# Kernel tuning notes

Measured on AMD Instinct MI355X. Metric: run time of the kernel, lower is better.

## Reference

```python
import jax, jax.numpy as jnp
import numpy as np

N, L, S, C, H = 8, 1024, 1024, 512, 8
SCALE = float((C // H) ** 0.5)  # sqrt(64), as in source (based on embed_dim, not cat'd dim)


def _linear_params(key, c_in, c_out):
    kw, kb = jax.random.split(key)
    lim = 1.0 / np.sqrt(c_in)
    W = jax.random.uniform(kw, (c_out, c_in), jnp.float32, -lim, lim)
    b = jax.random.uniform(kb, (c_out,), jnp.float32, -lim, lim)
    return W, b


def setup_inputs() -> dict:
    key = jax.random.key(0)
    ks = jax.random.split(key, 12)
    inp = {
        'q_c': jax.random.normal(ks[0], (N, L, C), jnp.float32),
        'q_p': jax.random.normal(ks[1], (N, L, C), jnp.float32),
        'k_c': jax.random.normal(ks[2], (N, S, C), jnp.float32),
        'k_p': jax.random.normal(ks[3], (N, S, C), jnp.float32),
        'v': jax.random.normal(ks[4], (N, S, C), jnp.float32),
        'attn_mask': jax.random.normal(ks[5], (N, H, L, S), jnp.float32),
    }
    for i, name in enumerate(['qc', 'qp', 'kc', 'kp', 'v', 'o']):
        W, b = _linear_params(ks[6 + i], C, C)
        inp[f'W_{name}'] = W
        inp[f'b_{name}'] = b
    return inp


def _split_head(x, h):
    n, l, c = x.shape
    return x.reshape(n, l, h, c // h).transpose(0, 2, 1, 3)  # (N,H,L,c/h)


def reference(q_c, q_p, k_c, k_p, v, attn_mask,
              W_qc, b_qc, W_qp, b_qp, W_kc, b_kc, W_kp, b_kp, W_v, b_v, W_o, b_o):
    # dual projections + cat -> (N, L, 2C)
    q = jnp.concatenate([q_c @ W_qc.T + b_qc, q_p @ W_qp.T + b_qp], axis=-1)
    k = jnp.concatenate([k_c @ W_kc.T + b_kc, k_p @ W_kp.T + b_kp], axis=-1)
    vv = v @ W_v.T + b_v
    q = _split_head(q, H)   # (N,H,L,2C/H)
    k = _split_head(k, H)   # (N,H,S,2C/H)
    vv = _split_head(vv, H)  # (N,H,S,C/H)
    attn = jnp.einsum('nhld,nhsd->nhls', q / SCALE, k) + attn_mask
    attn = jax.nn.softmax(attn, axis=-1)
    out = jnp.einsum('nhls,nhsd->nhld', attn, vv)
    out = out.transpose(0, 2, 1, 3).reshape(N, L, C)
    return out @ W_o.T + b_o
```

## Files before the change

### kernel.cpp

```cpp
#include <hip/hip_runtime.h>
#include <hip/hip_bf16.h>

typedef __bf16 bf16;
typedef __bf16 bf16x8 __attribute__((ext_vector_type(8)));
typedef float  f32x4  __attribute__((ext_vector_type(4)));
typedef float  f32x2  __attribute__((ext_vector_type(2)));

#define LOG2E        1.4426950408889634f
#define QSCALE_LOG2E 0.18033688011112043f
#define DEFER_THR    20.0f

#define GLDS(g, l)                                                        \
  __builtin_amdgcn_global_load_lds(                                       \
      (const __attribute__((address_space(1))) void*)(g),                 \
      (__attribute__((address_space(3))) void*)(l), 16, 0, 0)

#define WAITV(n) asm volatile("s_waitcnt vmcnt(" #n ")" ::: "memory")
#define BARRIER() do {                                                    \
  __builtin_amdgcn_s_barrier();                                           \
  __builtin_amdgcn_sched_barrier(0);                                      \
} while (0)

__device__ __forceinline__ void stage_f32_tile(const float* __restrict__ src, int ld,
                                               char* dst, int tid) {
  #pragma unroll
  for (int t = 0; t < 8; ++t) {
    int c8  = tid + t * 256;
    int row = c8 >> 4;
    int h8  = c8 & 15;
    const f32x4 v = *reinterpret_cast<const f32x4*>(src + row * ld + h8 * 4);
    union { bf16 h[4]; unsigned long long u; } pk;
    pk.h[0] = (bf16)v[0]; pk.h[1] = (bf16)v[1];
    pk.h[2] = (bf16)v[2]; pk.h[3] = (bf16)v[3];
    int byte = (row << 7) + ((((h8 >> 1) ^ (row & 7)) << 4) | ((h8 & 1) << 3));
    *reinterpret_cast<unsigned long long*>(dst + byte) = pk.u;
  }
}

__device__ __forceinline__ void stage_bf16_tile(const bf16* __restrict__ src, int ld,
                                                char* dst, int tid) {
  #pragma unroll
  for (int t = 0; t < 4; ++t) {
    int c   = tid + t * 256;
    int row = c >> 3;
    int ck  = c & 7;
    const bf16x8 v = *reinterpret_cast<const bf16x8*>(src + row * ld + ck * 8);
    int byte = (row << 7) + (((ck ^ (row & 7)) << 4));
    *reinterpret_cast<bf16x8*>(dst + byte) = v;
  }
}

__global__ __launch_bounds__(256) void proj_gemm(
    const float* __restrict__ qc, const float* __restrict__ qp,
    const float* __restrict__ kc, const float* __restrict__ kp,
    const float* __restrict__ vin,
    const float* __restrict__ Wqc, const float* __restrict__ bqc,
    const float* __restrict__ Wqp, const float* __restrict__ bqp,
    const float* __restrict__ Wkc, const float* __restrict__ bkc,
    const float* __restrict__ Wkp, const float* __restrict__ bkp,
    const float* __restrict__ Wv,  const float* __restrict__ bv,
    bf16* __restrict__ Qws, bf16* __restrict__ Kws, bf16* __restrict__ Vtws) {
  __shared__ __align__(16) bf16 lA[128 * 64];
  __shared__ __align__(16) bf16 lB[128 * 64];
  char* lAb = (char*)lA;
  char* lBb = (char*)lB;

  const int bxr = blockIdx.x;
  const int bx  = (bxr & 7) * 160 + (bxr >> 3);
  const int g  = bx >> 8;
  const int mt = (bx & 255) >> 2;
  const int nt = bx & 3;

  const float *A, *W, *bias;
  if      (g == 0) { A = qc;  W = Wqc; bias = bqc; }
  else if (g == 1) { A = qp;  W = Wqp; bias = bqp; }
  else if (g == 2) { A = kc;  W = Wkc; bias = bkc; }
  else if (g == 3) { A = kp;  W = Wkp; bias = bkp; }
  else             { A = vin; W = Wv;  bias = bv;  }

  const int tid  = threadIdx.x;
  const int lane = tid & 63, wid = tid >> 6;
  const int wr = wid >> 1, wc = wid & 1;
  const int lrow = lane & 15, lgrp = lane >> 4;

  const float* Abase = A + (size_t)(mt * 128) * 512;
  const float* Wbase = W + (size_t)(nt * 128) * 512;

  const f32x4 fz = {0.f, 0.f, 0.f, 0.f};
  f32x4 acc[4][4];
  #pragma unroll
  for (int i = 0; i < 4; ++i)
    #pragma unroll
    for (int j = 0; j < 4; ++j) acc[i][j] = fz;

  for (int k0 = 0; k0 < 512; k0 += 64) {
    __syncthreads();
    stage_f32_tile(Abase + k0, 512, lAb, tid);
    stage_f32_tile(Wbase + k0, 512, lBb, tid);
    __syncthreads();
    #pragma unroll
    for (int kk = 0; kk < 2; ++kk) {
      bf16x8 af[4], bfr[4];
      #pragma unroll
      for (int mf = 0; mf < 4; ++mf) {
        int row  = wr * 64 + mf * 16 + lrow;
        int byte = (row << 7) + ((((kk << 2) | lgrp) ^ (row & 7)) << 4);
        af[mf] = *reinterpret_cast<const bf16x8*>(lAb + byte);
      }
      #pragma unroll
      for (int nf = 0; nf < 4; ++nf) {
        int row  = wc * 64 + nf * 16 + lrow;
        int byte = (row << 7) + ((((kk << 2) | lgrp) ^ (row & 7)) << 4);
        bfr[nf] = *reinterpret_cast<const bf16x8*>(lBb + byte);
      }
      #pragma unroll
      for (int mf = 0; mf < 4; ++mf)
        #pragma unroll
        for (int nf = 0; nf < 4; ++nf)
          acc[mf][nf] = __builtin_amdgcn_mfma_f32_16x16x32_bf16(
              af[mf], bfr[nf], acc[mf][nf], 0, 0, 0);
    }
  }

  float bcol[4];
  #pragma unroll
  for (int nf = 0; nf < 4; ++nf)
    bcol[nf] = bias[nt * 128 + wc * 64 + nf * 16 + lrow];

  #pragma unroll
  for (int mf = 0; mf < 4; ++mf) {
    #pragma unroll
    for (int nf = 0; nf < 4; ++nf) {
      #pragma unroll
      for (int r = 0; r < 4; ++r) {
        int grow = mt * 128 + wr * 64 + mf * 16 + lgrp * 4 + r;
        int col  = nt * 128 + wc * 64 + nf * 16 + lrow;
        float vv = acc[mf][nf][r] + bcol[nf];
        bf16 hb  = (bf16)vv;
        int n = grow >> 10, tt = grow & 1023;
        if (g < 2) {
          int j = (g << 9) + col;
          Qws[(size_t)((((n << 3) + (j >> 7)) << 10) | tt) * 128 + (j & 127)] = hb;
        } else if (g < 4) {
          int j = ((g - 2) << 9) + col;
          Kws[(size_t)((((n << 3) + (j >> 7)) << 10) | tt) * 128 + (j & 127)] = hb;
        } else {
          int h = col >> 6, d = col & 63;
          Vtws[(size_t)((((n << 3) + h) << 6) + d) * 1024 + tt] = hb;
        }
      }
    }
  }
}

__global__ __launch_bounds__(256) void attn_fwd(
    const bf16* __restrict__ Qws, const bf16* __restrict__ Kws,
    const bf16* __restrict__ Vtws, const float* __restrict__ mask,
    bf16* __restrict__ Ows) {
  __shared__ __align__(16) char Kl[2][8192];
  __shared__ __align__(16) char Vl[2][4096];
  __shared__ __align__(16) char Ml[5][8192];
  __shared__ __align__(16) char Pl[4][1024];

  const int bxr = blockIdx.x;
  const int bx  = (bxr & 7) * 128 + (bxr >> 3);
  const int nh = bx >> 4;
  const int qt = bx & 15;
  const int tid = threadIdx.x;
  const int lane = tid & 63, wid = tid >> 6;
  const int lrow = lane & 15, lgrp = lane >> 4;
  const int q0 = qt * 64 + wid * 16;

  const bf16* Qb = Qws + ((size_t)(nh * 1024 + q0 + lrow)) * 128 + lgrp * 8;
  bf16x8 qf[4];
  #pragma unroll
  for (int kk = 0; kk < 4; ++kk)
    qf[kk] = *reinterpret_cast<const bf16x8*>(Qb + kk * 32);

  const float* Mblk = mask + ((size_t)(nh * 1024) + qt * 64) * 1024;
  const float* Mg = Mblk + (size_t)(lane >> 3) * 1024 +
                    (((lane & 7) ^ (lane >> 3)) << 2);

  const bf16* sgp[4];
  char* sdp[4];
  int srcMul = 128, dstStride = 8192;
  if (wid == 1 || wid == 2) {
    #pragma unroll
    for (int jj = 0; jj < 4; ++jj) {
      int j = (wid - 1) * 4 + jj;
      int c = j * 64 + lane;
      int key = c >> 4, kd = c & 15;
      sgp[jj] = Kws + ((size_t)(nh * 1024 + key)) * 128 + (kd ^ ((key >> 1) & 7)) * 8;
      sdp[jj] = (char*)&Kl[0][0] + j * 1024;
    }
  } else if (wid == 3) {
    #pragma unroll
    for (int jj = 0; jj < 4; ++jj) {
      int c = jj * 64 + lane;
      int vr = c >> 2, vs = c & 3;
      sgp[jj] = Vtws + ((size_t)(nh * 64 + vr)) * 1024 + vs * 8;
      sdp[jj] = (char*)&Vl[0][0] + jj * 1024;
    }
    srcMul = 1; dstStride = 4096;
  }

  char* Pb = &Pl[wid][0];

  const f32x4 fz = {0.f, 0.f, 0.f, 0.f};
  f32x4 oacc[4];
  #pragma unroll
  for (int dt = 0; dt < 4; ++dt) oacc[dt] = fz;
  float m2[4], lsum[4];
  #pragma unroll
  for (int r = 0; r < 4; ++r) { m2[r] = 0.f; lsum[r] = 0.f; }

  auto stageM = [&](char* dst, int sN) {
    #pragma unroll
    for (int i = 0; i < 8; ++i)
      GLDS(Mg + i * 8192 + sN, dst + i * 1024);
  };
  auto stageKV = [&](int buf, int sN) {
    if (wid >= 1) {
      #pragma unroll
      for (int jj = 0; jj < 4; ++jj)
        GLDS(sgp[jj] + (size_t)sN * srcMul, sdp[jj] + buf * dstStride);
    }
  };

  auto compute = [&](const char* Kb, const char* Vb, const char* Mb) {
    bf16x8 kf0[4], kf1[4], vf[4];
    #pragma unroll
    for (int kk = 0; kk < 4; ++kk) {
      int cb = ((((kk << 2) | lgrp) ^ (lrow & 7)) << 4);
      kf0[kk] = *reinterpret_cast<const bf16x8*>(Kb + lrow * 512 + cb);
      kf1[kk] = *reinterpret_cast<const bf16x8*>(Kb + lrow * 512 + 256 + cb);
    }
    #pragma unroll
    for (int dt = 0; dt < 4; ++dt)
      vf[dt] = *reinterpret_cast<const bf16x8*>(Vb + (dt * 16 + lrow) * 64 + lgrp * 16);
    f32x2 mk[4];
    #pragma unroll
    for (int r = 0; r < 4; ++r) {
      int qrow = wid * 16 + lgrp * 4 + r;
      int mchunk = (lrow >> 1) ^ (qrow & 7);
      mk[r] = *reinterpret_cast<const f32x2*>(
          Mb + qrow * 128 + (mchunk << 4) + ((lrow & 1) << 3));
    }

    f32x4 sc0 = fz, sc1 = fz;
    __builtin_amdgcn_s_setprio(1);
    #pragma unroll
    for (int kk = 0; kk < 4; ++kk)
      sc0 = __builtin_amdgcn_mfma_f32_16x16x32_bf16(qf[kk], kf0[kk], sc0, 0, 0, 0);
    #pragma unroll
    for (int kk = 0; kk < 4; ++kk)
      sc1 = __builtin_amdgcn_mfma_f32_16x16x32_bf16(qf[kk], kf1[kk], sc1, 0, 0, 0);
    __builtin_amdgcn_s_setprio(0);

    float a0r[4], a1r[4];
    bool ok = true;
    #pragma unroll
    for (int r = 0; r < 4; ++r) {
      a0r[r] = fmaf(sc0[r], QSCALE_LOG2E, mk[r].x * LOG2E);
      a1r[r] = fmaf(sc1[r], QSCALE_LOG2E, mk[r].y * LOG2E);
      ok &= (fmaxf(a0r[r], a1r[r]) <= m2[r] + DEFER_THR);
    }
    if (__builtin_expect(!__all(ok), 0)) {
      #pragma unroll
      for (int r = 0; r < 4; ++r) {
        float tv = fmaxf(a0r[r], a1r[r]);
        tv = fmaxf(tv, __shfl_xor(tv, 1));
        tv = fmaxf(tv, __shfl_xor(tv, 2));
        tv = fmaxf(tv, __shfl_xor(tv, 4));
        tv = fmaxf(tv, __shfl_xor(tv, 8));
        float mn = fmaxf(m2[r], tv);
        float corr = exp2f(m2[r] - mn);
        m2[r] = mn;
        lsum[r] *= corr;
        #pragma unroll
        for (int dt = 0; dt < 4; ++dt) oacc[dt][r] *= corr;
      }
    }
    #pragma unroll
    for (int r = 0; r < 4; ++r) {
      float e0 = exp2f(a0r[r] - m2[r]);
      float e1 = exp2f(a1r[r] - m2[r]);
      lsum[r] += e0 + e1;
      union { bf16 h[2]; unsigned u; } pk;
      pk.h[0] = (bf16)e0; pk.h[1] = (bf16)e1;
      int row = lgrp * 4 + r;
      int byte = row * 64 + ((((lrow >> 2) ^ (row & 3)) << 4) | ((lrow & 3) << 2));
      *reinterpret_cast<unsigned*>(Pb + byte) = pk.u;
    }
    __builtin_amdgcn_wave_barrier();
    __builtin_amdgcn_sched_barrier(0);
    bf16x8 pf = *reinterpret_cast<const bf16x8*>(
        Pb + lrow * 64 + ((lgrp ^ (lrow & 3)) << 4));

    __builtin_amdgcn_s_setprio(1);
    #pragma unroll
    for (int dt = 0; dt < 4; ++dt)
      oacc[dt] = __builtin_amdgcn_mfma_f32_16x16x32_bf16(pf, vf[dt], oacc[dt], 0, 0, 0);
    __builtin_amdgcn_s_setprio(0);
  };

  char *mr0 = &Ml[0][0], *mr1 = &Ml[1][0], *mr2 = &Ml[2][0],
       *mr3 = &Ml[3][0], *mr4 = &Ml[4][0];
  auto rotM = [&]() {
    char* tp = mr0; mr0 = mr1; mr1 = mr2; mr2 = mr3; mr3 = mr4; mr4 = tp;
  };

  if (wid == 0) {
    stageM(mr0, 0); stageM(mr1, 32); stageM(mr2, 64); stageM(mr3, 96);
  } else {
    stageKV(0, 0);
  }
  if (wid == 0) { WAITV(24); } else { WAITV(0); }
  BARRIER();

  for (int t = 0; t < 28; ++t) {
    if (wid == 0) stageM(mr4, (t + 4) * 32);
    else          stageKV((t + 1) & 1, (t + 1) * 32);
    compute(&Kl[t & 1][0], &Vl[t & 1][0], mr0);
    if (wid == 0) { WAITV(24); } else { WAITV(0); }
    BARRIER();
    rotM();
  }
  stageKV(1, 29 * 32);
  compute(&Kl[0][0], &Vl[0][0], mr0);
  if (wid == 0) { WAITV(16); } else { WAITV(0); }
  BARRIER(); rotM();

  stageKV(0, 30 * 32);
  compute(&Kl[1][0], &Vl[1][0], mr0);
  if (wid == 0) { WAITV(8); } else { WAITV(0); }
  BARRIER(); rotM();

  stageKV(1, 31 * 32);
  compute(&Kl[0][0], &Vl[0][0], mr0);
  WAITV(0);
  BARRIER(); rotM();

  compute(&Kl[1][0], &Vl[1][0], mr0);

  #pragma unroll
  for (int r = 0; r < 4; ++r) {
    float ss = lsum[r];
    ss += __shfl_xor(ss, 1);
    ss += __shfl_xor(ss, 2);
    ss += __shfl_xor(ss, 4);
    ss += __shfl_xor(ss, 8);
    lsum[r] = 1.0f / ss;
  }

  const int n = nh >> 3, h = nh & 7;
  bf16* Ob = Ows + ((size_t)(n * 1024 + q0 + lgrp * 4)) * 512 + h * 64 + lrow;
  #pragma unroll
  for (int dt = 0; dt < 4; ++dt)
    #pragma unroll
    for (int r = 0; r < 4; ++r)
      Ob[(size_t)r * 512 + dt * 16] = (bf16)(oacc[dt][r] * lsum[r]);
}

__global__ __launch_bounds__(256) void out_gemm(
    const bf16* __restrict__ Ows, const float* __restrict__ Wo,
    const float* __restrict__ bo, float* __restrict__ out) {
  __shared__ __align__(16) bf16 lA[128 * 64];
  __shared__ __align__(16) bf16 lB[128 * 64];
  char* lAb = (char*)lA;
  char* lBb = (char*)lB;

  const int bxr = blockIdx.x;
  const int bx  = (bxr & 7) * 32 + (bxr >> 3);
  const int mt = bx >> 2;
  const int nt = bx & 3;
  const int tid = threadIdx.x;
  const int lane = tid & 63, wid = tid >> 6;
  const int wr = wid >> 1, wc = wid & 1;
  const int lrow = lane & 15, lgrp = lane >> 4;

  const bf16*  Abase = Ows + (size_t)(mt * 128) * 512;
  const float* Wbase = Wo  + (size_t)(nt * 128) * 512;

  const f32x4 fz = {0.f, 0.f, 0.f, 0.f};
  f32x4 acc[4][4];
  #pragma unroll
  for (int i = 0; i < 4; ++i)
    #pragma unroll
    for (int j = 0; j < 4; ++j) acc[i][j] = fz;

  for (int k0 = 0; k0 < 512; k0 += 64) {
    __syncthreads();
    stage_bf16_tile(Abase + k0, 512, lAb, tid);
    stage_f32_tile(Wbase + k0, 512, lBb, tid);
    __syncthreads();
    #pragma unroll
    for (int kk = 0; kk < 2; ++kk) {
      bf16x8 af[4], bfr[4];
      #pragma unroll
      for (int mf = 0; mf < 4; ++mf) {
        int row  = wr * 64 + mf * 16 + lrow;
        int byte = (row << 7) + ((((kk << 2) | lgrp) ^ (row & 7)) << 4);
        af[mf] = *reinterpret_cast<const bf16x8*>(lAb + byte);
      }
      #pragma unroll
      for (int nf = 0; nf < 4; ++nf) {
        int row  = wc * 64 + nf * 16 + lrow;
        int byte = (row << 7) + ((((kk << 2) | lgrp) ^ (row & 7)) << 4);
        bfr[nf] = *reinterpret_cast<const bf16x8*>(lBb + byte);
      }
      #pragma unroll
      for (int mf = 0; mf < 4; ++mf)
        #pragma unroll
        for (int nf = 0; nf < 4; ++nf)
          acc[mf][nf] = __builtin_amdgcn_mfma_f32_16x16x32_bf16(
              af[mf], bfr[nf], acc[mf][nf], 0, 0, 0);
    }
  }

  float bcol[4];
  #pragma unroll
  for (int nf = 0; nf < 4; ++nf)
    bcol[nf] = bo[nt * 128 + wc * 64 + nf * 16 + lrow];

  #pragma unroll
  for (int mf = 0; mf < 4; ++mf) {
    #pragma unroll
    for (int nf = 0; nf < 4; ++nf) {
      #pragma unroll
      for (int r = 0; r < 4; ++r) {
        int grow = mt * 128 + wr * 64 + mf * 16 + lgrp * 4 + r;
        int col  = nt * 128 + wc * 64 + nf * 16 + lrow;
        out[(size_t)grow * 512 + col] = acc[mf][nf][r] + bcol[nf];
      }
    }
  }
}

extern "C" void kernel_launch(void* const* d_in, const int* in_sizes, int n_in,
                              void* d_out, int out_size, void* d_ws, size_t ws_size,
                              hipStream_t stream) {
  const float* qc   = (const float*)d_in[0];
  const float* qp   = (const float*)d_in[1];
  const float* kc   = (const float*)d_in[2];
  const float* kp   = (const float*)d_in[3];
  const float* vin  = (const float*)d_in[4];
  const float* mask = (const float*)d_in[5];
  const float* Wqc  = (const float*)d_in[6];
  const float* bqc  = (const float*)d_in[7];
  const float* Wqp  = (const float*)d_in[8];
  const float* bqp  = (const float*)d_in[9];
  const float* Wkc  = (const float*)d_in[10];
  const float* bkc  = (const float*)d_in[11];
  const float* Wkp  = (const float*)d_in[12];
  const float* bkp  = (const float*)d_in[13];
  const float* Wv   = (const float*)d_in[14];
  const float* bv   = (const float*)d_in[15];
  const float* Wo   = (const float*)d_in[16];
  const float* bo   = (const float*)d_in[17];

  bf16* Qws  = (bf16*)d_ws;
  bf16* Kws  = Qws  + (size_t)8 * 1024 * 1024;
  bf16* Vtws = Kws  + (size_t)8 * 1024 * 1024;
  bf16* Ows  = Vtws + (size_t)4 * 1024 * 1024;

  proj_gemm<<<dim3(1280), dim3(256), 0, stream>>>(
      qc, qp, kc, kp, vin, Wqc, bqc, Wqp, bqp, Wkc, bkc, Wkp, bkp, Wv, bv,
      Qws, Kws, Vtws);
  attn_fwd<<<dim3(1024), dim3(256), 0, stream>>>(Qws, Kws, Vtws, mask, Ows);
  out_gemm<<<dim3(256), dim3(256), 0, stream>>>(Ows, Wo, bo, (float*)d_out);
}
```

Baseline: 200.6 us.

## Triple-buffer K/V tiles with pre-swizzled contiguous global layouts in attention

The projection epilogue now writes K and V-transposed into tile-contiguous, pre-swizzled layouts, so the attention kernel's K/V staging becomes straight linear global-to-LDS copies. K/V LDS buffers go from double to triple buffering, with loads issued two tiles ahead and a partial vmcnt wait instead of a full drain. The mask staging drops its XOR swizzle and is read linearly. This is meant to hide K/V load latency and simplify address math, at the cost of more LDS (which may reduce occupancy) and possible bank conflicts on the unswizzled mask reads.

```diff
diff --git a/kernel.cpp b/kernel.cpp
--- a/kernel.cpp
+++ b/kernel.cpp
@@ -142,11 +142,15 @@
           int j = (g << 9) + col;
           Qws[(size_t)((((n << 3) + (j >> 7)) << 10) | tt) * 128 + (j & 127)] = hb;
         } else if (g < 4) {
-          int j = ((g - 2) << 9) + col;
-          Kws[(size_t)((((n << 3) + (j >> 7)) << 10) | tt) * 128 + (j & 127)] = hb;
+          int j  = ((g - 2) << 9) + col;
+          int hh = j >> 7, d = j & 127;
+          int dd = (((d >> 3) ^ ((tt >> 1) & 7)) << 3) | (d & 7);
+          Kws[(size_t)((((n << 3) + hh) << 10) | tt) * 128 + dd] = hb;
         } else {
           int h = col >> 6, d = col & 63;
-          Vtws[(size_t)((((n << 3) + h) << 6) + d) * 1024 + tt] = hb;
+          int kt2 = tt >> 5, si = tt & 31;
+          int ss = (((si >> 3) ^ ((d >> 1) & 3)) << 3) | (si & 7);
+          Vtws[((size_t)((((n << 3) + h) << 5) + kt2) * 64 + d) * 32 + ss] = hb;
         }
       }
     }
@@ -157,8 +161,8 @@
     const bf16* __restrict__ Qws, const bf16* __restrict__ Kws,
     const bf16* __restrict__ Vtws, const float* __restrict__ mask,
     bf16* __restrict__ Ows) {
-  __shared__ __align__(16) char Kl[2][8192];
-  __shared__ __align__(16) char Vl[2][4096];
+  __shared__ __align__(16) char Kl[3][8192];
+  __shared__ __align__(16) char Vl[3][4096];
   __shared__ __align__(16) char Ml[5][8192];
   __shared__ __align__(16) char Pl[4][1024];
 
@@ -177,32 +181,10 @@
   for (int kk = 0; kk < 4; ++kk)
     qf[kk] = *reinterpret_cast<const bf16x8*>(Qb + kk * 32);
 
-  const float* Mblk = mask + ((size_t)(nh * 1024) + qt * 64) * 1024;
-  const float* Mg = Mblk + (size_t)(lane >> 3) * 1024 +
-                    (((lane & 7) ^ (lane >> 3)) << 2);
-
-  const bf16* sgp[4];
-  char* sdp[4];
-  int srcMul = 128, dstStride = 8192;
-  if (wid == 1 || wid == 2) {
-    #pragma unroll
-    for (int jj = 0; jj < 4; ++jj) {
-      int j = (wid - 1) * 4 + jj;
-      int c = j * 64 + lane;
-      int key = c >> 4, kd = c & 15;
-      sgp[jj] = Kws + ((size_t)(nh * 1024 + key)) * 128 + (kd ^ ((key >> 1) & 7)) * 8;
-      sdp[jj] = (char*)&Kl[0][0] + j * 1024;
-    }
-  } else if (wid == 3) {
-    #pragma unroll
-    for (int jj = 0; jj < 4; ++jj) {
-      int c = jj * 64 + lane;
-      int vr = c >> 2, vs = c & 3;
-      sgp[jj] = Vtws + ((size_t)(nh * 64 + vr)) * 1024 + vs * 8;
-      sdp[jj] = (char*)&Vl[0][0] + jj * 1024;
-    }
-    srcMul = 1; dstStride = 4096;
-  }
+  const float* Mg = mask + ((size_t)(nh * 1024) + qt * 64 + (lane >> 3)) * 1024 +
+                    (lane & 7) * 4;
+  const bf16* Kg = Kws + (size_t)nh * 131072 + lane * 8;
+  const bf16* Vg = Vtws + (size_t)nh * 65536 + lane * 8;
 
   char* Pb = &Pl[wid][0];
 
@@ -214,16 +196,23 @@
   #pragma unroll
   for (int r = 0; r < 4; ++r) { m2[r] = 0.f; lsum[r] = 0.f; }
 
-  auto stageM = [&](char* dst, int sN) {
-    #pragma unroll
-    for (int i = 0; i < 8; ++i)
-      GLDS(Mg + i * 8192 + sN, dst + i * 1024);
+  auto stageM = [&](char* dst, int kt) {
+    if (wid == 0) {
+      #pragma unroll
+      for (int i = 0; i < 8; ++i)
+        GLDS(Mg + i * 8192 + kt * 32, dst + i * 1024);
+    }
   };
-  auto stageKV = [&](int buf, int sN) {
-    if (wid >= 1) {
-      #pragma unroll
-      for (int jj = 0; jj < 4; ++jj)
-        GLDS(sgp[jj] + (size_t)sN * srcMul, sdp[jj] + buf * dstStride);
+  auto stageKV = [&](char* Kd, char* Vd, int kt) {
+    if (wid == 1 || wid == 2) {
+      #pragma unroll
+      for (int j = 0; j < 4; ++j)
+        GLDS(Kg + kt * 4096 + (wid - 1) * 2048 + j * 512,
+             Kd + (wid - 1) * 4096 + j * 1024);
+    } else if (wid == 3) {
+      #pragma unroll
+      for (int j = 0; j < 4; ++j)
+        GLDS(Vg + kt * 2048 + j * 512, Vd + j * 1024);
     }
   };
 
@@ -237,14 +226,13 @@
     }
     #pragma unroll
     for (int dt = 0; dt < 4; ++dt)
-      vf[dt] = *reinterpret_cast<const bf16x8*>(Vb + (dt * 16 + lrow) * 64 + lgrp * 16);
+      vf[dt] = *reinterpret_cast<const bf16x8*>(
+          Vb + (dt * 16 + lrow) * 64 + ((lgrp ^ ((lrow >> 1) & 3)) << 4));
     f32x2 mk[4];
     #pragma unroll
     for (int r = 0; r < 4; ++r) {
       int qrow = wid * 16 + lgrp * 4 + r;
-      int mchunk = (lrow >> 1) ^ (qrow & 7);
-      mk[r] = *reinterpret_cast<const f32x2*>(
-          Mb + qrow * 128 + (mchunk << 4) + ((lrow & 1) << 3));
+      mk[r] = *reinterpret_cast<const f32x2*>(Mb + qrow * 128 + lrow * 8);
     }
 
     f32x4 sc0 = fz, sc1 = fz;
@@ -304,44 +292,47 @@
     __builtin_amdgcn_s_setprio(0);
   };
 
-  char *mr0 = &Ml[0][0], *mr1 = &Ml[1][0], *mr2 = &Ml[2][0],
-       *mr3 = &Ml[3][0], *mr4 = &Ml[4][0];
+  char *ka = &Kl[0][0], *kb2 = &Kl[1][0], *kc2 = &Kl[2][0];
+  char *va = &Vl[0][0], *vb2 = &Vl[1][0], *vc2 = &Vl[2][0];
+  char *m0 = &Ml[0][0], *m1 = &Ml[1][0], *m2p = &Ml[2][0],
+       *m3 = &Ml[3][0], *m4 = &Ml[4][0];
+  auto rotKV = [&]() {
+    char* tp = ka; ka = kb2; kb2 = kc2; kc2 = tp;
+    tp = va; va = vb2; vb2 = vc2; vc2 = tp;
+  };
   auto rotM = [&]() {
-    char* tp = mr0; mr0 = mr1; mr1 = mr2; mr2 = mr3; mr3 = mr4; mr4 = tp;
+    char* tp = m0; m0 = m1; m1 = m2p; m2p = m3; m3 = m4; m4 = tp;
   };
 
-  if (wid == 0) {
-    stageM(mr0, 0); stageM(mr1, 32); stageM(mr2, 64); stageM(mr3, 96);
-  } else {
-    stageKV(0, 0);
-  }
-  if (wid == 0) { WAITV(24); } else { WAITV(0); }
+  stageKV(ka, va, 0);
+  stageKV(kb2, vb2, 1);
+  stageM(m0, 0); stageM(m1, 1); stageM(m2p, 2); stageM(m3, 3);
+  if (wid == 0) { WAITV(24); } else { WAITV(4); }
   BARRIER();
 
   for (int t = 0; t < 28; ++t) {
-    if (wid == 0) stageM(mr4, (t + 4) * 32);
-    else          stageKV((t + 1) & 1, (t + 1) * 32);
-    compute(&Kl[t & 1][0], &Vl[t & 1][0], mr0);
-    if (wid == 0) { WAITV(24); } else { WAITV(0); }
+    stageKV(kc2, vc2, t + 2);
+    stageM(m4, t + 4);
+    compute(ka, va, m0);
+    if (wid == 0) { WAITV(24); } else { WAITV(4); }
     BARRIER();
-    rotM();
-  }
-  stageKV(1, 29 * 32);
-  compute(&Kl[0][0], &Vl[0][0], mr0);
-  if (wid == 0) { WAITV(16); } else { WAITV(0); }
-  BARRIER(); rotM();
-
-  stageKV(0, 30 * 32);
-  compute(&Kl[1][0], &Vl[1][0], mr0);
-  if (wid == 0) { WAITV(8); } else { WAITV(0); }
-  BARRIER(); rotM();
-
-  stageKV(1, 31 * 32);
-  compute(&Kl[0][0], &Vl[0][0], mr0);
+    rotKV(); rotM();
+  }
+  stageKV(kc2, vc2, 30);
+  compute(ka, va, m0);
+  if (wid == 0) { WAITV(16); } else { WAITV(4); }
+  BARRIER(); rotKV(); rotM();
+
+  stageKV(kc2, vc2, 31);
+  compute(ka, va, m0);
+  if (wid == 0) { WAITV(8); } else { WAITV(4); }
+  BARRIER(); rotKV(); rotM();
+
+  compute(ka, va, m0);
   WAITV(0);
-  BARRIER(); rotM();
-
-  compute(&Kl[1][0], &Vl[1][0], mr0);
+  BARRIER(); rotKV(); rotM();
+
+  compute(ka, va, m0);
 
   #pragma unroll
   for (int r = 0; r < 4; ++r) {
```

Result: faster. 183.9 us (-8.3%).
